# Optimization experiments

Hardware: AMD Instinct MI355X
Metric: run time of the kernel (lower is better)

## Reference

```python
import jax, jax.numpy as jnp
import numpy as np


def lstm_step(x_t, h, c, Wih, Whh, bih, bhh):
    # PyTorch LSTM gate order: i, f, g, o
    gates = x_t @ Wih.T + h @ Whh.T + bih + bhh
    i, f, g, o = jnp.split(gates, 4, axis=-1)
    i = jax.nn.sigmoid(i)
    f = jax.nn.sigmoid(f)
    g = jnp.tanh(g)
    o = jax.nn.sigmoid(o)
    c_new = f * c + i * g
    h_new = o * jnp.tanh(c_new)
    return h_new, c_new


def setup_inputs() -> dict:
    key = jax.random.key(0)
    N, C, T, V, M = 512, 3, 300, 25, 2
    F = C * V * M  # 150
    H = 100
    ks = jax.random.split(key, 12)
    s = 1.0 / np.sqrt(H)  # PyTorch LSTM/Linear init scale
    u = lambda k, shape: jax.random.uniform(k, shape, jnp.float32, -s, s)
    return {
        "x": jax.random.normal(ks[0], (N, C, T, V, M), jnp.float32),
        "enc_Wih": u(ks[1], (4 * H, F)),
        "enc_Whh": u(ks[2], (4 * H, H)),
        "enc_bih": u(ks[3], (4 * H,)),
        "enc_bhh": u(ks[4], (4 * H,)),
        "dec_Wih": u(ks[5], (4 * H, F)),
        "dec_Whh": u(ks[6], (4 * H, H)),
        "dec_bih": u(ks[7], (4 * H,)),
        "dec_bhh": u(ks[8], (4 * H,)),
        "fc_W": u(ks[9], (F, H)),
        "fc_b": u(ks[10], (F,)),
    }


def reference(x, enc_Wih, enc_Whh, enc_bih, enc_bhh,
              dec_Wih, dec_Whh, dec_bih, dec_bhh, fc_W, fc_b):
    N, C, T, V, M = x.shape
    F = C * V * M
    H = enc_Whh.shape[1]
    # (N,C,T,V,M) -> (N,T,C*V*M)
    xs = jnp.transpose(x, (0, 2, 1, 3, 4)).reshape(N, T, F)

    # Encoder LSTM: only need final (h, c)
    h0 = jnp.zeros((N, H), x.dtype)
    c0 = jnp.zeros((N, H), x.dtype)

    def enc_step(carry, xt):
        h, c = carry
        h, c = lstm_step(xt, h, c, enc_Wih, enc_Whh, enc_bih, enc_bhh)
        return (h, c), None

    (h, c), _ = jax.lax.scan(enc_step, (h0, c0), jnp.swapaxes(xs, 0, 1))

    inp0 = jnp.zeros((N, F), x.dtype)

    def dec_step(carry, _):
        inp, h, c = carry
        h, c = lstm_step(inp, h, c, dec_Wih, dec_Whh, dec_bih, dec_bhh)
        out = h @ fc_W.T + fc_b
        return (out, h, c), out

    _, outs = jax.lax.scan(dec_step, (inp0, h, c), None, length=T - 1)  # [T-1,N,F]

    # outputs[:,0,:] stays zero, like the torch.zeros buffer
    outputs = jnp.concatenate([jnp.zeros((1, N, F), x.dtype), outs], axis=0)  # [T,N,F]
    outputs = jnp.swapaxes(outputs, 0, 1).reshape(N, T, C, V, M)
    return jnp.transpose(outputs, (0, 2, 1, 3, 4))  # (N,C,T,V,M)
```

## Files before the change

kernel.cpp:

```cpp
#include <hip/hip_runtime.h>
#include <hip/hip_fp16.h>


#define B_W2P   0u
#define B_WDP   102400u
#define B_WEP   204800u
#define B_PIH   307200u
#define B_BENC  460800u
#define B_B1    462848u
#define B_BEFF  464896u
#define B_HIST  466944u
#define HIST_STRIDE 29952

typedef _Float16 h2_t __attribute__((ext_vector_type(2)));
typedef _Float16 f16x8 __attribute__((ext_vector_type(8)));
typedef float f32x4v __attribute__((ext_vector_type(4)));

#if defined(__has_builtin)
#if __has_builtin(__builtin_amdgcn_fdot2)
#define HAS_FDOT2 1
#endif
#endif

__device__ __forceinline__ float fdot2u(unsigned a, unsigned b, float c) {
#ifdef HAS_FDOT2
  return __builtin_amdgcn_fdot2(__builtin_bit_cast(h2_t, a), __builtin_bit_cast(h2_t, b), c, false);
#else
  float al = __half2float(__ushort_as_half((unsigned short)(a & 0xffffu)));
  float ah = __half2float(__ushort_as_half((unsigned short)(a >> 16)));
  float bl = __half2float(__ushort_as_half((unsigned short)(b & 0xffffu)));
  float bh = __half2float(__ushort_as_half((unsigned short)(b >> 16)));
  return fmaf(ah, bh, fmaf(al, bl, c));
#endif
}

__device__ __forceinline__ unsigned pack2f(float a, float b) {
  return (unsigned)__half_as_ushort(__float2half(a)) |
         ((unsigned)__half_as_ushort(__float2half(b)) << 16);
}

__device__ __forceinline__ float fast_sig(float x) {
  float e = __builtin_amdgcn_exp2f(x * -1.442695040888963f);
  return __builtin_amdgcn_rcpf(1.f + e);
}
__device__ __forceinline__ float fast_tanh(float x) {
  float e = __builtin_amdgcn_exp2f(x * -2.885390081777926f);
  return fmaf(2.f, __builtin_amdgcn_rcpf(1.f + e), -1.f);
}

__device__ __forceinline__ f32x4v mfma16(uint4 a, uint4 b, f32x4v c) {
  return __builtin_amdgcn_mfma_f32_16x16x32_f16(
      __builtin_bit_cast(f16x8, a), __builtin_bit_cast(f16x8, b), c, 0, 0, 0);
}

__global__ void prep(const float* __restrict__ dWih, const float* __restrict__ dWhh,
                     const float* __restrict__ dbih, const float* __restrict__ dbhh,
                     const float* __restrict__ eWih, const float* __restrict__ eWhh,
                     const float* __restrict__ ebih, const float* __restrict__ ebhh,
                     const float* __restrict__ fcW,  const float* __restrict__ fcb,
                     char* __restrict__ wsb)
{
  int idx = blockIdx.x * 256 + threadIdx.x;
  if (idx < 25600) {
    int q = idx >> 9, t = idx & 511;
    unsigned w2p = 0, wdp = 0, wep = 0;
    if (t < 400) {
      int r = (t & 3) * 100 + (t >> 2);
      int j0 = 2 * q, j1 = 2 * q + 1;
      float wd0 = dWhh[r * 100 + j0], wd1 = dWhh[r * 100 + j1];
      float we0 = eWhh[r * 100 + j0], we1 = eWhh[r * 100 + j1];
      float s0 = 0.f, s1 = 0.f;
      for (int f = 0; f < 150; ++f) {
        float a = dWih[r * 150 + f];
        s0 = fmaf(a, fcW[f * 100 + j0], s0);
        s1 = fmaf(a, fcW[f * 100 + j1], s1);
      }
      w2p = pack2f(wd0 + s0, wd1 + s1);
      wdp = pack2f(wd0, wd1);
      wep = pack2f(we0, we1);
    }
    ((unsigned*)(wsb + B_W2P))[idx] = w2p;
    ((unsigned*)(wsb + B_WDP))[idx] = wdp;
    ((unsigned*)(wsb + B_WEP))[idx] = wep;
  } else if (idx < 25600 + 38400) {
    int k = idx - 25600; int d = k >> 9, t = k & 511;
    unsigned pk = 0;
    if (t < 400) {
      int r = (t & 3) * 100 + (t >> 2);
      pk = pack2f(eWih[r * 150 + 2 * d], eWih[r * 150 + 2 * d + 1]);
    }
    ((unsigned*)(wsb + B_PIH))[k] = pk;
  } else if (idx < 25600 + 38400 + 512) {
    int t = idx - (25600 + 38400);
    float be = 0.f, b1 = 0.f, bf = 0.f;
    if (t < 400) {
      int r = (t & 3) * 100 + (t >> 2);
      be = ebih[r] + ebhh[r];
      b1 = dbih[r] + dbhh[r];
      float acc = 0.f;
      for (int f = 0; f < 150; ++f) acc = fmaf(dWih[r * 150 + f], fcb[f], acc);
      bf = b1 + acc;
    }
    ((float*)(wsb + B_BENC))[t] = be;
    ((float*)(wsb + B_B1))[t]   = b1;
    ((float*)(wsb + B_BEFF))[t] = bf;
  }
}

__global__ __launch_bounds__(448, 2)
void recurrent(const float* __restrict__ x, char* __restrict__ wsb)
{
  const int tid  = threadIdx.x;
  const int w    = tid >> 6;
  const int lane = tid & 63;
  const int sp   = lane & 15;
  const int q    = lane >> 4;
  const int nb   = blockIdx.x * 16;

  __shared__ unsigned short hx[2][16][264];
  for (int k = tid; k < 2 * 16 * 264; k += 448) ((unsigned short*)hx)[k] = 0;

  const unsigned* WEP = (const unsigned*)(wsb + B_WEP);
  const unsigned* WDP = (const unsigned*)(wsb + B_WDP);
  const unsigned* W2P = (const unsigned*)(wsb + B_W2P);
  const unsigned* PIH = (const unsigned*)(wsb + B_PIH);

  const int nt = (w < 4) ? 4 : 3;
  int cells[4];
  float4 bs[4];
  uint4 af[4][8];
#pragma unroll
  for (int i = 0; i < 4; ++i) {
    const int tile = (i < nt) ? (w + 7 * i) : 0;
    const int col = tile * 16 + sp;
    cells[i] = 4 * tile + q;
#pragma unroll
    for (int kk = 0; kk < 8; ++kk) {
      unsigned e[4];
#pragma unroll
      for (int l = 0; l < 4; ++l) {
        const int p = kk * 16 + q * 4 + l;
        unsigned v = 0u;
        if (p < 50) v = WEP[p * 512 + col];
        else if (p < 125) v = PIH[(p - 50) * 512 + col];
        e[l] = v;
      }
      af[i][kk] = make_uint4(e[0], e[1], e[2], e[3]);
    }
    bs[i] = ((const float4*)(wsb + B_BENC))[cells[i]];
  }

  const bool stg = tid < 400;
  const int ssp = tid / 25;
  const int sr  = tid - ssp * 25;
  const float* xb = x + (size_t)(nb + (stg ? ssp : 0)) * 45000;
  int soff[6];
#pragma unroll
  for (int l = 0; l < 6; ++l) {
    const int f = sr * 6 + l;
    const int cd = f / 50;
    soff[l] = cd * 15000 + (f - cd * 50);
  }
  const int sdst = (stg ? ssp : 0) * 264 + 100 + sr * 6;

  unsigned short* histn = (unsigned short*)(wsb + B_HIST) + (size_t)(nb + sp) * HIST_STRIDE;

  __syncthreads();
  if (stg) {
    float xv[6];
#pragma unroll
    for (int l = 0; l < 6; ++l) xv[l] = xb[soff[l]];
    unsigned short* d = &hx[0][0][0] + sdst;
    *(unsigned*)(d + 0) = pack2f(xv[0], xv[1]);
    *(unsigned*)(d + 2) = pack2f(xv[2], xv[3]);
    *(unsigned*)(d + 4) = pack2f(xv[4], xv[5]);
  }
  __syncthreads();

  float cst[4] = {0.f, 0.f, 0.f, 0.f};

  for (int t = 0; t < 300; ++t) {
    const int rd = t & 1, wr = rd ^ 1;
    const bool pf = stg && (t < 299);
    float xv[6];
    if (pf) {
      const int to = (t + 1) * 50;
#pragma unroll
      for (int l = 0; l < 6; ++l) xv[l] = xb[soff[l] + to];
    }
    f32x4v acc[4];
#pragma unroll
    for (int i = 0; i < 4; ++i) {
      acc[i][0] = bs[i].x; acc[i][1] = bs[i].y;
      acc[i][2] = bs[i].z; acc[i][3] = bs[i].w;
    }
#pragma unroll
    for (int kk = 0; kk < 8; ++kk) {
      uint4 b = *(const uint4*)(&hx[rd][sp][kk * 32 + q * 8]);
#pragma unroll
      for (int i = 0; i < 4; ++i)
        if (i < nt) acc[i] = mfma16(af[i][kk], b, acc[i]);
    }
#pragma unroll
    for (int i = 0; i < 4; ++i) {
      if (i < nt) {
        float ii = fast_sig(acc[i][0]), ff = fast_sig(acc[i][1]);
        float gg = fast_tanh(acc[i][2]), oo = fast_sig(acc[i][3]);
        cst[i] = fmaf(ff, cst[i], ii * gg);
        float h = oo * fast_tanh(cst[i]);
        hx[wr][sp][cells[i]] = __half_as_ushort(__float2half(h));
      }
    }
    if (pf) {
      unsigned short* d = &hx[wr][0][0] + sdst;
      *(unsigned*)(d + 0) = pack2f(xv[0], xv[1]);
      *(unsigned*)(d + 2) = pack2f(xv[2], xv[3]);
      *(unsigned*)(d + 4) = pack2f(xv[4], xv[5]);
    }
    __syncthreads();
  }

  auto loadA4 = [&](const unsigned* W, unsigned bofs) {
#pragma unroll
    for (int i = 0; i < 4; ++i) {
      const int tile = (i < nt) ? (w + 7 * i) : 0;
      const int col = tile * 16 + sp;
#pragma unroll
      for (int kk = 0; kk < 4; ++kk) {
        unsigned e[4];
#pragma unroll
        for (int l = 0; l < 4; ++l) {
          const int p = kk * 16 + q * 4 + l;
          e[l] = (p < 50) ? W[p * 512 + col] : 0u;
        }
        af[i][kk] = make_uint4(e[0], e[1], e[2], e[3]);
      }
      bs[i] = ((const float4*)(wsb + bofs))[cells[i]];
    }
  };

  loadA4(WDP, B_B1);
  {
    f32x4v acc[4];
#pragma unroll
    for (int i = 0; i < 4; ++i) {
      acc[i][0] = bs[i].x; acc[i][1] = bs[i].y;
      acc[i][2] = bs[i].z; acc[i][3] = bs[i].w;
    }
#pragma unroll
    for (int kk = 0; kk < 4; ++kk) {
      uint4 b = *(const uint4*)(&hx[0][sp][kk * 32 + q * 8]);
#pragma unroll
      for (int i = 0; i < 4; ++i)
        if (i < nt) acc[i] = mfma16(af[i][kk], b, acc[i]);
    }
#pragma unroll
    for (int i = 0; i < 4; ++i) {
      if (i < nt) {
        float ii = fast_sig(acc[i][0]), ff = fast_sig(acc[i][1]);
        float gg = fast_tanh(acc[i][2]), oo = fast_sig(acc[i][3]);
        cst[i] = fmaf(ff, cst[i], ii * gg);
        float h = oo * fast_tanh(cst[i]);
        hx[1][sp][cells[i]] = __half_as_ushort(__float2half(h));
        histn[cells[i]] = __half_as_ushort(__float2half(h));
      }
    }
    __syncthreads();
  }
  loadA4(W2P, B_BEFF);
  for (int s = 2; s <= 299; ++s) {
    const int rd = (299 + s) & 1, wr = rd ^ 1;
    f32x4v acc[4];
#pragma unroll
    for (int i = 0; i < 4; ++i) {
      acc[i][0] = bs[i].x; acc[i][1] = bs[i].y;
      acc[i][2] = bs[i].z; acc[i][3] = bs[i].w;
    }
#pragma unroll
    for (int kk = 0; kk < 4; ++kk) {
      uint4 b = *(const uint4*)(&hx[rd][sp][kk * 32 + q * 8]);
#pragma unroll
      for (int i = 0; i < 4; ++i)
        if (i < nt) acc[i] = mfma16(af[i][kk], b, acc[i]);
    }
#pragma unroll
    for (int i = 0; i < 4; ++i) {
      if (i < nt) {
        float ii = fast_sig(acc[i][0]), ff = fast_sig(acc[i][1]);
        float gg = fast_tanh(acc[i][2]), oo = fast_sig(acc[i][3]);
        cst[i] = fmaf(ff, cst[i], ii * gg);
        float h = oo * fast_tanh(cst[i]);
        hx[wr][sp][cells[i]] = __half_as_ushort(__float2half(h));
        histn[(s - 1) * 100 + cells[i]] = __half_as_ushort(__float2half(h));
      }
    }
    __syncthreads();
  }
}

__global__ __launch_bounds__(192, 4)
void emit(const char* __restrict__ wsb, const float* __restrict__ fcW,
          const float* __restrict__ fcb, float* __restrict__ out)
{
  const int f = threadIdx.x;
  const int n = blockIdx.x;
  const int z = blockIdx.y;
  __shared__ unsigned short hl[15008];

  const uint4* src = (const uint4*)((const unsigned short*)(wsb + B_HIST) +
                                    (size_t)n * HIST_STRIDE + z * 15000);
  for (int k = f; k < 1875; k += 192) ((uint4*)hl)[k] = src[k];

  const bool on = f < 150;
  unsigned fw[50];
  float bias = 0.f;
  if (on) {
    const float* fp = fcW + f * 100;
#pragma unroll
    for (int q = 0; q < 50; ++q) fw[q] = pack2f(fp[2 * q], fp[2 * q + 1]);
    bias = fcb[f];
  }
  __syncthreads();

  if (!on) return;
  const int cc = f / 50, r = f - cc * 50;
  float* ob = out + (size_t)n * 45000 + cc * 15000 + r;
  if (z == 0) ob[0] = 0.f;
  const int rows = z ? 149 : 150;
  for (int tl = 0; tl < rows; ++tl) {
    const uint4* row = (const uint4*)(hl + tl * 100);
    float a0 = bias, a1 = 0.f, a2 = 0.f, a3 = 0.f;
#pragma unroll
    for (int ch = 0; ch < 12; ++ch) {
      uint4 v = row[ch];
      a0 = fdot2u(fw[4 * ch + 0], v.x, a0);
      a1 = fdot2u(fw[4 * ch + 1], v.y, a1);
      a2 = fdot2u(fw[4 * ch + 2], v.z, a2);
      a3 = fdot2u(fw[4 * ch + 3], v.w, a3);
    }
    uint2 v2 = *(const uint2*)(hl + tl * 100 + 96);
    a0 = fdot2u(fw[48], v2.x, a0);
    a1 = fdot2u(fw[49], v2.y, a1);
    const int tt = z * 150 + tl + 1;
    ob[tt * 50] = (a0 + a1) + (a2 + a3);
  }
}

extern "C" void kernel_launch(void* const* d_in, const int* in_sizes, int n_in,
                              void* d_out, int out_size, void* d_ws, size_t ws_size,
                              hipStream_t stream) {
  const float* x    = (const float*)d_in[0];
  const float* eWih = (const float*)d_in[1];
  const float* eWhh = (const float*)d_in[2];
  const float* ebih = (const float*)d_in[3];
  const float* ebhh = (const float*)d_in[4];
  const float* dWih = (const float*)d_in[5];
  const float* dWhh = (const float*)d_in[6];
  const float* dbih = (const float*)d_in[7];
  const float* dbhh = (const float*)d_in[8];
  const float* fcW  = (const float*)d_in[9];
  const float* fcb  = (const float*)d_in[10];
  float* out = (float*)d_out;
  char* wsb  = (char*)d_ws;

  prep<<<252, 256, 0, stream>>>(dWih, dWhh, dbih, dbhh, eWih, eWhh, ebih, ebhh, fcW, fcb, wsb);
  recurrent<<<32, 448, 0, stream>>>(x, wsb);
  emit<<<dim3(512, 2), 192, 0, stream>>>(wsb, fcW, fcb, out);
}
```

Measured before the change: 1.200 ms.

## Use eight waves per recurrent block and prefetch inputs two steps ahead

The recurrent kernel moves from 7 to 8 waves per block, so the 25 gate tiles are spread with at most 4 per wave (only wave 0 takes 4) instead of 4 on four of the waves. The input staging becomes a two-step software pipeline. The step t+1 input is written to shared memory at the start of the iteration, and the global load for step t+2 is issued before the MFMA work, giving the load a whole iteration to land. This costs extra registers and a larger block. The launch bound drops the minimum of 2 blocks per CU, which changes the register budget.

```diff
diff --git a/kernel.cpp b/kernel.cpp
--- a/kernel.cpp
+++ b/kernel.cpp
@@ -107,7 +107,7 @@
   }
 }
 
-__global__ __launch_bounds__(448, 2)
+__global__ __launch_bounds__(512)
 void recurrent(const float* __restrict__ x, char* __restrict__ wsb)
 {
   const int tid  = threadIdx.x;
@@ -118,20 +118,20 @@
   const int nb   = blockIdx.x * 16;
 
   __shared__ unsigned short hx[2][16][264];
-  for (int k = tid; k < 2 * 16 * 264; k += 448) ((unsigned short*)hx)[k] = 0;
+  for (int k = tid; k < 2 * 16 * 264; k += 512) ((unsigned short*)hx)[k] = 0;
 
   const unsigned* WEP = (const unsigned*)(wsb + B_WEP);
   const unsigned* WDP = (const unsigned*)(wsb + B_WDP);
   const unsigned* W2P = (const unsigned*)(wsb + B_W2P);
   const unsigned* PIH = (const unsigned*)(wsb + B_PIH);
 
-  const int nt = (w < 4) ? 4 : 3;
+  const int nt = (w == 0) ? 4 : 3;
   int cells[4];
   float4 bs[4];
   uint4 af[4][8];
 #pragma unroll
   for (int i = 0; i < 4; ++i) {
-    const int tile = (i < nt) ? (w + 7 * i) : 0;
+    const int tile = (i < nt) ? (w + 8 * i) : 0;
     const int col = tile * 16 + sp;
     cells[i] = 4 * tile + q;
 #pragma unroll
@@ -166,14 +166,17 @@
   unsigned short* histn = (unsigned short*)(wsb + B_HIST) + (size_t)(nb + sp) * HIST_STRIDE;
 
   __syncthreads();
+  float xW[6];
   if (stg) {
-    float xv[6];
-#pragma unroll
-    for (int l = 0; l < 6; ++l) xv[l] = xb[soff[l]];
+    float x0[6];
+#pragma unroll
+    for (int l = 0; l < 6; ++l) x0[l] = xb[soff[l]];
     unsigned short* d = &hx[0][0][0] + sdst;
-    *(unsigned*)(d + 0) = pack2f(xv[0], xv[1]);
-    *(unsigned*)(d + 2) = pack2f(xv[2], xv[3]);
-    *(unsigned*)(d + 4) = pack2f(xv[4], xv[5]);
+    *(unsigned*)(d + 0) = pack2f(x0[0], x0[1]);
+    *(unsigned*)(d + 2) = pack2f(x0[2], x0[3]);
+    *(unsigned*)(d + 4) = pack2f(x0[4], x0[5]);
+#pragma unroll
+    for (int l = 0; l < 6; ++l) xW[l] = xb[soff[l] + 50];
   }
   __syncthreads();
 
@@ -181,12 +184,17 @@
 
   for (int t = 0; t < 300; ++t) {
     const int rd = t & 1, wr = rd ^ 1;
-    const bool pf = stg && (t < 299);
-    float xv[6];
-    if (pf) {
-      const int to = (t + 1) * 50;
-#pragma unroll
-      for (int l = 0; l < 6; ++l) xv[l] = xb[soff[l] + to];
+    if (stg && t < 299) {
+      unsigned short* d = &hx[wr][0][0] + sdst;
+      *(unsigned*)(d + 0) = pack2f(xW[0], xW[1]);
+      *(unsigned*)(d + 2) = pack2f(xW[2], xW[3]);
+      *(unsigned*)(d + 4) = pack2f(xW[4], xW[5]);
+    }
+    float xL[6];
+    if (stg && t < 298) {
+      const int to = (t + 2) * 50;
+#pragma unroll
+      for (int l = 0; l < 6; ++l) xL[l] = xb[soff[l] + to];
     }
     f32x4v acc[4];
 #pragma unroll
@@ -211,19 +219,17 @@
         hx[wr][sp][cells[i]] = __half_as_ushort(__float2half(h));
       }
     }
-    if (pf) {
-      unsigned short* d = &hx[wr][0][0] + sdst;
-      *(unsigned*)(d + 0) = pack2f(xv[0], xv[1]);
-      *(unsigned*)(d + 2) = pack2f(xv[2], xv[3]);
-      *(unsigned*)(d + 4) = pack2f(xv[4], xv[5]);
-    }
     __syncthreads();
+    if (stg) {
+#pragma unroll
+      for (int l = 0; l < 6; ++l) xW[l] = xL[l];
+    }
   }
 
   auto loadA4 = [&](const unsigned* W, unsigned bofs) {
 #pragma unroll
     for (int i = 0; i < 4; ++i) {
-      const int tile = (i < nt) ? (w + 7 * i) : 0;
+      const int tile = (i < nt) ? (w + 8 * i) : 0;
       const int col = tile * 16 + sp;
 #pragma unroll
       for (int kk = 0; kk < 4; ++kk) {
@@ -364,6 +370,6 @@
   char* wsb  = (char*)d_ws;
 
   prep<<<252, 256, 0, stream>>>(dWih, dWhh, dbih, dbhh, eWih, eWhh, ebih, ebhh, fcW, fcb, wsb);
-  recurrent<<<32, 448, 0, stream>>>(x, wsb);
+  recurrent<<<32, 512, 0, stream>>>(x, wsb);
   emit<<<dim3(512, 2), 192, 0, stream>>>(wsb, fcW, fcb, out);
 }
```

Result: no change. 1.217 ms (+1.4%).
